# Performance work log

Measured on AMD Instinct MI355X. Metric: run time of the kernel, lower is better.

Reference implementation:

```python
import jax, jax.numpy as jnp
import numpy as np
from jax import lax

WINDOW_SIZE = 5
SIGMA = 1.0
DILATIONS = [1 + int(i ** 1.5) for i in range(5)]  # [1, 2, 3, 6, 9]
C1 = (0.01 * 255.0) ** 2
C2 = (0.03 * 255.0) ** 2


def _make_window(channel=1):
    x = np.arange(WINDOW_SIZE, dtype=np.float64)
    g = np.exp(-((x - WINDOW_SIZE // 2) ** 2) / (2.0 * SIGMA ** 2))
    g = g / g.sum()
    w2d = np.outer(g, g)
    w2d = w2d / w2d.sum()
    w = np.broadcast_to(w2d[None, None], (channel, 1, WINDOW_SIZE, WINDOW_SIZE))
    return jnp.asarray(w, jnp.float32)


def _dw_conv(x, window, dilation):
    # depthwise 'same' conv; pad = (dilated_kernel - 1)/2 = 2*dilation (always even total pad)
    pad = 2 * dilation
    return lax.conv_general_dilated(
        x, window, window_strides=(1, 1),
        padding=((pad, pad), (pad, pad)),
        rhs_dilation=(dilation, dilation),
        dimension_numbers=('NCHW', 'OIHW', 'NCHW'),
        feature_group_count=window.shape[0])


def _ssim_mean(img1, img2, window, dilation):
    mu1 = _dw_conv(img1, window, dilation)
    mu2 = _dw_conv(img2, window, dilation)
    si11 = _dw_conv(img1 * img1, window, dilation)
    si22 = _dw_conv(img2 * img2, window, dilation)
    si12 = _dw_conv(img1 * img2, window, dilation)
    mu1_sq = mu1 * mu1
    mu2_sq = mu2 * mu2
    mu1_mu2 = mu1 * mu2
    sigma1_sq = si11 - mu1_sq
    sigma2_sq = si22 - mu2_sq
    sigma12 = si12 - mu1_mu2
    ssim_map = ((2.0 * mu1_mu2 + C1) * (2.0 * sigma12 + C2)) / (
        (mu1_sq + mu2_sq + C1) * (sigma1_sq + sigma2_sq + C2))
    return jnp.mean(ssim_map)


def _avg_pool2(x):
    B, C, H, W = x.shape
    return x.reshape(B, C, H // 2, 2, W // 2, 2).mean(axis=(3, 5))


def setup_inputs() -> dict:
    key = jax.random.key(0)
    k1, k2 = jax.random.split(key)
    img1 = jax.random.uniform(k1, (16, 1, 1024, 1024), dtype=jnp.float32)
    img2 = jax.random.uniform(k2, (16, 1, 1024, 1024), dtype=jnp.float32)
    window = _make_window(channel=1)
    weights = jnp.asarray([0.0448, 0.2856, 0.3001, 0.2363, 0.1333], jnp.float32)
    return {"img1": img1, "img2": img2, "window": window, "weights": weights}


def reference(img1, img2, window, weights):
    eps = 1e-12
    m = jnp.max(img2)
    a = (img1 + eps) / (m + eps) * 255.0
    b = (img2 + eps) / (m + eps) * 255.0
    mssim = []
    for dil in DILATIONS:
        mssim.append(_ssim_mean(a, b, window, dil))
        a = _avg_pool2(a)
        b = _avg_pool2(b)
    mssim = jnp.stack(mssim)
    return 1.0 - jnp.prod(mssim ** weights)
```

## Files before the change

### kernel.cpp

```cpp
#include <hip/hip_runtime.h>
#include <math.h>

#define EPSN 1e-12f
#define SSIM_C1 6.5025f
#define SSIM_C2 58.5225f


typedef __attribute__((ext_vector_type(2))) float vf2;
typedef __attribute__((ext_vector_type(2))) _Float16 h2;
typedef __attribute__((ext_vector_type(8))) _Float16 h8;

__device__ __forceinline__ vf2 h2f(h2 v) { return vf2{(float)v.x, (float)v.y}; }


__global__ void init_ws_kernel(float* ws) {
    if (threadIdx.x < 16) ws[threadIdx.x] = 0.0f;
}


__global__ void max_kernel(const float4* __restrict__ img2, int n4,
                           unsigned* __restrict__ maxbits) {
    float m = 0.0f;
    for (int i = blockIdx.x * blockDim.x + threadIdx.x; i < n4;
         i += gridDim.x * blockDim.x) {
        float4 v = img2[i];
        m = fmaxf(fmaxf(m, fmaxf(v.x, v.y)), fmaxf(v.z, v.w));
    }
#pragma unroll
    for (int o = 32; o > 0; o >>= 1) m = fmaxf(m, __shfl_down(m, o));
    __shared__ float sm[4];
    int tid = threadIdx.x;
    if ((tid & 63) == 0) sm[tid >> 6] = m;
    __syncthreads();
    if (tid == 0) {
        float mm = fmaxf(fmaxf(sm[0], sm[1]), fmaxf(sm[2], sm[3]));
        atomicMax(maxbits, __float_as_uint(mm));
    }
}


__device__ __forceinline__ float ssim_px(vf2 vpm, vf2 vsq, float s2h) {
    float u = vpm.x * vpm.x, vv = vpm.y * vpm.y;
    float upv = u + vv, umv = u - vv;
    float qp = vsq.x + vsq.y, qm = vsq.x - vsq.y;
    float num1 = fmaf(s2h, umv, SSIM_C1);
    float den1 = fmaf(s2h, upv, SSIM_C1);
    float num2 = fmaf(s2h, qm - umv, SSIM_C2);
    float den2 = fmaf(s2h, qp - upv, SSIM_C2);
    return (num1 * num2) * __builtin_amdgcn_rcpf(den1 * den2);
}

__device__ __forceinline__ void load_g1(const float* __restrict__ window,
                                        float* g1) {
#pragma unroll
    for (int k = 0; k < 5; k++)
        g1[k] = ((window[k * 5 + 0] + window[k * 5 + 1]) +
                 (window[k * 5 + 2] + window[k * 5 + 3])) + window[k * 5 + 4];
}

__device__ __forceinline__ void block_sum_add(float local, float* part, int tid,
                                              float* __restrict__ sumOut) {
#pragma unroll
    for (int o = 32; o > 0; o >>= 1) local += __shfl_down(local, o);
    if ((tid & 63) == 0) part[tid >> 6] = local;
    __syncthreads();
    if (tid == 0)
        atomicAdd(sumOut, (part[0] + part[1]) + (part[2] + part[3]));
}

template <int D, int TPT, int LW, int L0>
__device__ __forceinline__ float sep_compute(const h2* AB, const float* g1,
                                             float s2h, int tx, int ty) {
    vf2 rPM[5], rSQ[5];
    float local = 0.0f;
    int rbase = ty * TPT;
#pragma unroll
    for (int ph = 0; ph < D; ++ph) {
        const int cnt = (TPT - ph + D - 1) / D;
#pragma unroll
        for (int k = 0; k < cnt + 4; ++k) {
            const h2* row = AB + (rbase + ph + k * D) * LW + (L0 - 2 * D) + tx;
            vf2 hpm = {0, 0}, hsq = {0, 0};
#pragma unroll
            for (int kt = 0; kt < 5; kt++) {
                vf2 f = h2f(row[kt * D]);
                vf2 w = g1[kt] * f;
                hpm += w;
                hsq += w * f;
            }
            rPM[k % 5] = hpm;
            rSQ[k % 5] = hsq;
            if (k >= 4) {
                vf2 vpm = {0, 0}, vsq = {0, 0};
#pragma unroll
                for (int kt = 0; kt < 5; kt++) {
                    int sl = (k - 4 + kt) % 5;
                    vpm += g1[kt] * rPM[sl];
                    vsq += g1[kt] * rSQ[sl];
                }
                local += ssim_px(vpm, vsq, s2h);
            }
        }
    }
    return local;
}

template <int D, int LH, int LW, int L0, int W>
__device__ __forceinline__ void stage_h2(const h2* __restrict__ base, h2* AB,
                                         int x0i, int y0, int tid) {
    for (int idx = tid; idx < LH * 16; idx += 256) {
        int ly = idx >> 4, j = idx & 15;
        int gy = y0 + ly;
        float4 g = make_float4(0, 0, 0, 0);
        if ((unsigned)gy < (unsigned)W)
            g = *(const float4*)(base + (size_t)gy * W + x0i + 4 * j);
        *(float4*)&AB[ly * LW + L0 + 4 * j] = g;
    }
    for (int idx = tid; idx < LH * 4 * D; idx += 256) {
        int ly = idx / (4 * D), h = idx % (4 * D);
        int gc = (h < 2 * D) ? h : h + 64;
        int gx = x0i - 2 * D + gc, gy = y0 + ly;
        h2 pm = {(_Float16)0.f, (_Float16)0.f};
        if ((unsigned)gx < (unsigned)W && (unsigned)gy < (unsigned)W)
            pm = base[(size_t)gy * W + gx];
        AB[ly * LW + (L0 - 2 * D) + gc] = pm;
    }
}


__global__ __launch_bounds__(256) void ssim0_kernel(
        const float* __restrict__ A, const float* __restrict__ B,
        const float* __restrict__ window, const unsigned* __restrict__ maxbits,
        float* __restrict__ sums, h2* __restrict__ pm1) {
    constexpr int TH = 64, TPT = 16, L0 = 4, LW = 72, LH = 68;
    __shared__ __align__(16) h2 AB[LH * LW];
    __shared__ float part[4];

    int tx = threadIdx.x, ty = threadIdx.y;
    int tid = ty * 64 + tx;
    int b = blockIdx.z;
    int x0i = blockIdx.x * 64;
    int y0 = blockIdx.y * TH - 2;

    const float* Ab = A + (size_t)b * 1024 * 1024;
    const float* Bb = B + (size_t)b * 1024 * 1024;
    for (int idx = tid; idx < LH * 16; idx += 256) {
        int ly = idx >> 4, j = idx & 15;
        int gy = y0 + ly;
        float4 a = make_float4(0, 0, 0, 0), v = make_float4(0, 0, 0, 0);
        if ((unsigned)gy < 1024u) {
            a = *(const float4*)(Ab + (size_t)gy * 1024 + x0i + 4 * j);
            v = *(const float4*)(Bb + (size_t)gy * 1024 + x0i + 4 * j);
        }
        h8 r;
        r[0] = (_Float16)(a.x + v.x); r[1] = (_Float16)(a.x - v.x);
        r[2] = (_Float16)(a.y + v.y); r[3] = (_Float16)(a.y - v.y);
        r[4] = (_Float16)(a.z + v.z); r[5] = (_Float16)(a.z - v.z);
        r[6] = (_Float16)(a.w + v.w); r[7] = (_Float16)(a.w - v.w);
        *(h8*)&AB[ly * LW + L0 + 4 * j] = r;
    }
    for (int idx = tid; idx < LH * 4; idx += 256) {
        int ly = idx >> 2, h = idx & 3;
        int gc = (h < 2) ? h : h + 64;
        int gx = x0i - 2 + gc, gy = y0 + ly;
        h2 pm = {(_Float16)0.f, (_Float16)0.f};
        if ((unsigned)gx < 1024u && (unsigned)gy < 1024u) {
            float a = Ab[(size_t)gy * 1024 + gx], v = Bb[(size_t)gy * 1024 + gx];
            pm = h2{(_Float16)(a + v), (_Float16)(a - v)};
        }
        AB[ly * LW + (L0 - 2) + gc] = pm;
    }
    __syncthreads();

    {
        int py = tid >> 3, j4 = tid & 7;
        const h2* r0 = AB + (2 + 2 * py) * LW + L0 + 8 * j4;
        const h2* r1 = r0 + LW;
        h2 q = {(_Float16)0.25f, (_Float16)0.25f};
        h8 o;
#pragma unroll
        for (int t = 0; t < 4; t++) {
            h2 s = ((r0[2 * t] + r0[2 * t + 1]) + (r1[2 * t] + r1[2 * t + 1])) * q;
            o[2 * t] = s.x; o[2 * t + 1] = s.y;
        }
        int gx = (x0i >> 1) + 4 * j4, gy = blockIdx.y * 32 + py;
        *(h8*)(pm1 + (size_t)b * 512 * 512 + (size_t)gy * 512 + gx) = o;
    }

    float g1[5];
    load_g1(window, g1);
    float mx = __uint_as_float(*maxbits);
    float sc = 255.0f / (mx + EPSN);
    float s2h = 0.5f * sc * sc;

    float local = sep_compute<1, TPT, LW, L0>(AB, g1, s2h, tx, ty);
    block_sum_add(local, part, tid, sums + 0);
}


__global__ __launch_bounds__(256) void ssim1_kernel(
        const h2* __restrict__ pm1, const float* __restrict__ window,
        const unsigned* __restrict__ maxbits, float* __restrict__ sums,
        h2* __restrict__ pm2, h2* __restrict__ pm3, h2* __restrict__ pm4) {
    constexpr int D = 2, TH = 64, TPT = 16, L0 = 4, LW = 72, LH = 72;
    __shared__ __align__(16) h2 AB[LH * LW];
    __shared__ float part[4];

    int tx = threadIdx.x, ty = threadIdx.y;
    int tid = ty * 64 + tx;
    int b = blockIdx.z, bx = blockIdx.x, by = blockIdx.y;
    int x0i = bx * 64, y0 = by * TH - 4;
    const h2* base = pm1 + (size_t)b * 512 * 512;

    stage_h2<D, LH, LW, L0, 512>(base, AB, x0i, y0, tid);
    __syncthreads();

    {
        int py = tid >> 3, j4 = tid & 7;
        const h2* r0 = AB + (4 + 2 * py) * LW + 4 + 8 * j4;
        const h2* r1 = r0 + LW;
        h2 q = {(_Float16)0.25f, (_Float16)0.25f};
        h8 o;
#pragma unroll
        for (int t = 0; t < 4; t++) {
            h2 s = ((r0[2 * t] + r0[2 * t + 1]) + (r1[2 * t] + r1[2 * t + 1])) * q;
            o[2 * t] = s.x; o[2 * t + 1] = s.y;
        }
        int gx = bx * 32 + 4 * j4, gy = by * 32 + py;
        *(h8*)(pm2 + (size_t)b * 256 * 256 + (size_t)gy * 256 + gx) = o;
    }
    {
        int py = tid >> 4, px = tid & 15;
        h2 acc = {(_Float16)0.f, (_Float16)0.f};
#pragma unroll
        for (int ry = 0; ry < 4; ry++)
#pragma unroll
            for (int rx = 0; rx < 4; rx++)
                acc += AB[(4 + 4 * py + ry) * LW + 4 + 4 * px + rx];
        h2 q = {(_Float16)0.0625f, (_Float16)0.0625f};
        acc *= q;
        pm3[(size_t)b * 128 * 128 + (size_t)(by * 16 + py) * 128 + bx * 16 + px] = acc;
    }
    if (tid < 64) {
        int py = tid >> 3, px = tid & 7;
        h2 acc = {(_Float16)0.f, (_Float16)0.f};
#pragma unroll
        for (int ry = 0; ry < 8; ry++)
#pragma unroll
            for (int rx = 0; rx < 8; rx++)
                acc += AB[(4 + 8 * py + ry) * LW + 4 + 8 * px + rx];
        h2 q = {(_Float16)0.015625f, (_Float16)0.015625f};
        acc *= q;
        pm4[(size_t)b * 64 * 64 + (size_t)(by * 8 + py) * 64 + bx * 8 + px] = acc;
    }

    float g1[5];
    load_g1(window, g1);
    float mx = __uint_as_float(*maxbits);
    float sc = 255.0f / (mx + EPSN);
    float s2h = 0.5f * sc * sc;

    float local = sep_compute<D, TPT, LW, L0>(AB, g1, s2h, tx, ty);
    block_sum_add(local, part, tid, sums + 1);
}


template <int D, int TW, int TH, int W, int LW, int LH>
__device__ void direct_level(const h2* __restrict__ base, const float* g1,
                             int bx, int by, float s2h, float* part,
                             float* __restrict__ sumOut, h2* AB, int tid) {
    constexpr int NOUT = TW * TH / 256;
    int x0 = bx * TW - 2 * D, y0 = by * TH - 2 * D;

    for (int idx = tid; idx < LW * LH; idx += 256) {
        int ly = idx / LW, lx = idx - ly * LW;
        int px = x0 + lx, py = y0 + ly;
        h2 pm = {(_Float16)0.f, (_Float16)0.f};
        if ((unsigned)px < (unsigned)W && (unsigned)py < (unsigned)W)
            pm = base[(size_t)py * W + px];
        AB[idx] = pm;
    }
    __syncthreads();

    vf2 mu[NOUT], sq[NOUT];
#pragma unroll
    for (int j = 0; j < NOUT; j++) { mu[j] = vf2{0, 0}; sq[j] = vf2{0, 0}; }
#pragma unroll
    for (int ky = 0; ky < 5; ky++) {
#pragma unroll
        for (int kx = 0; kx < 5; kx++) {
            float w = g1[ky] * g1[kx];
#pragma unroll
            for (int j = 0; j < NOUT; j++) {
                int lin = tid + j * 256;
                int ox = lin % TW, oy = lin / TW;
                vf2 f = h2f(AB[(oy + ky * D) * LW + ox + kx * D]);
                vf2 wf = w * f;
                mu[j] += wf;
                sq[j] += wf * f;
            }
        }
    }
    float local = 0.0f;
#pragma unroll
    for (int j = 0; j < NOUT; j++) local += ssim_px(mu[j], sq[j], s2h);
    block_sum_add(local, part, tid, sumOut);
}

__global__ __launch_bounds__(256) void tail_kernel(
        const h2* __restrict__ pm2, const h2* __restrict__ pm3,
        const h2* __restrict__ pm4, const float* __restrict__ window,
        const unsigned* __restrict__ maxbits, float* __restrict__ sums,
        unsigned* __restrict__ counter, const float* __restrict__ weights,
        unsigned* __restrict__ out) {
    extern __shared__ __align__(16) h2 ldsdyn[];
    __shared__ float part[4];
    int tid = threadIdx.x;

    float g1[5];
    load_g1(window, g1);
    float mx = __uint_as_float(*maxbits);
    float sc = 255.0f / (mx + EPSN);
    float s2h = 0.5f * sc * sc;

    int bid = blockIdx.x;
    if (bid < 512) {
        int b = bid >> 5, r = bid & 31, by = r >> 2, bx = r & 3;
        constexpr int D = 3, TPT = 8, L0 = 8, LW = 80, LH = 44;
        const h2* base = pm2 + (size_t)b * 256 * 256;
        stage_h2<D, LH, LW, L0, 256>(base, ldsdyn, bx * 64, by * 32 - 6, tid);
        __syncthreads();
        float local = sep_compute<D, TPT, LW, L0>(ldsdyn, g1, s2h,
                                                  tid & 63, tid >> 6);
        block_sum_add(local, part, tid, sums + 2);
    } else if (bid < 768) {
        int t = bid - 512, b = t >> 4, r = t & 15, by = r >> 1, bx = r & 1;
        const h2* base = pm3 + (size_t)b * 128 * 128;
        direct_level<6, 64, 16, 128, 88, 40>(base, g1, bx, by, s2h, part,
                                             sums + 3, ldsdyn, tid);
    } else {
        int t = bid - 768, b = t >> 3, r = t & 7, by = r >> 1, bx = r & 1;
        const h2* base = pm4 + (size_t)b * 64 * 64;
        direct_level<9, 32, 16, 64, 68, 52>(base, g1, bx, by, s2h, part,
                                            sums + 4, ldsdyn, tid);
    }

    if (tid == 0) {
        __threadfence();
        if (atomicAdd(counter, 1u) == 895u) {
            __threadfence();
            const float counts[5] = {16.0f * 1024 * 1024, 16.0f * 512 * 512,
                                     16.0f * 256 * 256,   16.0f * 128 * 128,
                                     16.0f * 64 * 64};
            float prod = 1.0f;
#pragma unroll
            for (int i = 0; i < 5; i++) {
                float m = atomicAdd(sums + i, 0.0f) / counts[i];
                prod *= powf(m, weights[i]);
            }
            float r = 1.0f - prod;
            unsigned bits = __float_as_uint(r);
            unsigned lsb = (bits >> 16) & 1u;
            unsigned hi = (bits + 0x7FFFu + lsb) >> 16;
            out[0] = (hi << 16) | hi;
        }
    }
}


extern "C" void kernel_launch(void* const* d_in, const int* in_sizes, int n_in,
                              void* d_out, int out_size, void* d_ws, size_t ws_size,
                              hipStream_t stream) {
    const float* img1 = (const float*)d_in[0];
    const float* img2 = (const float*)d_in[1];
    const float* window = (const float*)d_in[2];
    const float* weights = (const float*)d_in[3];

    float* ws = (float*)d_ws;
    unsigned* maxbits = (unsigned*)d_ws;
    float* sums = ws + 4;
    unsigned* counter = (unsigned*)(ws + 10);
    size_t off = 512;
    h2* pm1 = (h2*)(ws + off); off += (size_t)16 * 512 * 512;
    h2* pm2 = (h2*)(ws + off); off += (size_t)16 * 256 * 256;
    h2* pm3 = (h2*)(ws + off); off += (size_t)16 * 128 * 128;
    h2* pm4 = (h2*)(ws + off); off += (size_t)16 * 64 * 64;

    init_ws_kernel<<<1, 64, 0, stream>>>(ws);
    max_kernel<<<2048, 256, 0, stream>>>((const float4*)img2,
                                         16 * 1024 * 1024 / 4, maxbits);
    ssim0_kernel<<<dim3(16, 16, 16), dim3(64, 4), 0, stream>>>(
        img1, img2, window, maxbits, sums, pm1);
    ssim1_kernel<<<dim3(8, 8, 16), dim3(64, 4), 0, stream>>>(
        pm1, window, maxbits, sums, pm2, pm3, pm4);
    tail_kernel<<<896, 256, 14144, stream>>>(pm2, pm3, pm4, window, maxbits,
                                             sums, counter, weights,
                                             (unsigned*)d_out);
}
```

Baseline: 279.1 us.

## Register-block separable SSIM with packed fp16 horizontal pass and smaller tiles

Replaces the per-thread column-strip separable convolution with a 4-column by 2-row register-blocked version. Each thread loads a row span with 16-byte LDS reads and does the horizontal 5-tap filter in packed fp16 (h2) arithmetic. It then scatters the results into fp32 vertical accumulators. Tile heights are halved (64→32 rows), doubling grid size, and LDS padding/offsets are adjusted. The intent is fewer LDS loads and packed-math throughput, at the cost of more halo overhead and reduced fp16 precision in the horizontal sums (including squared terms).

```diff
diff --git a/kernel.cpp b/kernel.cpp
--- a/kernel.cpp
+++ b/kernel.cpp
@@ -8,7 +8,9 @@
 
 typedef __attribute__((ext_vector_type(2))) float vf2;
 typedef __attribute__((ext_vector_type(2))) _Float16 h2;
+typedef __attribute__((ext_vector_type(4))) _Float16 h4;
 typedef __attribute__((ext_vector_type(8))) _Float16 h8;
+typedef __attribute__((ext_vector_type(4))) unsigned int u32x4;
 
 __device__ __forceinline__ vf2 h2f(h2 v) { return vf2{(float)v.x, (float)v.y}; }
 
@@ -51,11 +53,13 @@
 }
 
 __device__ __forceinline__ void load_g1(const float* __restrict__ window,
-                                        float* g1) {
-#pragma unroll
-    for (int k = 0; k < 5; k++)
+                                        float* g1, h2* g1h) {
+#pragma unroll
+    for (int k = 0; k < 5; k++) {
         g1[k] = ((window[k * 5 + 0] + window[k * 5 + 1]) +
                  (window[k * 5 + 2] + window[k * 5 + 3])) + window[k * 5 + 4];
+        g1h[k] = h2{(_Float16)g1[k], (_Float16)g1[k]};
+    }
 }
 
 __device__ __forceinline__ void block_sum_add(float local, float* part, int tid,
@@ -68,40 +72,70 @@
         atomicAdd(sumOut, (part[0] + part[1]) + (part[2] + part[3]));
 }
 
-template <int D, int TPT, int LW, int L0>
-__device__ __forceinline__ float sep_compute(const h2* AB, const float* g1,
-                                             float s2h, int tx, int ty) {
-    vf2 rPM[5], rSQ[5];
+template <int D, int RPT, int LW, int L0>
+__device__ __forceinline__ float sep4_compute(const h2* AB, const float* g1,
+                                              const h2* g1h, float s2h,
+                                              int cg, int rg) {
+    constexpr int SPAN = 4 * D + 4;
+    constexpr int NW = SPAN / 4;
+    constexpr int NIR = RPT + 4 * D;
+
+    vf2 apm[RPT][4], asq[RPT][4];
+#pragma unroll
+    for (int j = 0; j < RPT; j++)
+#pragma unroll
+        for (int c = 0; c < 4; c++) {
+            apm[j][c] = vf2{0.f, 0.f};
+            asq[j][c] = vf2{0.f, 0.f};
+        }
+
+    const h2* base = AB + (L0 - 2 * D) + 4 * cg + (rg * RPT) * LW;
+#pragma unroll
+    for (int i = 0; i < NIR; i++) {
+        h2 f[SPAN];
+#pragma unroll
+        for (int w = 0; w < NW; w++) {
+            u32x4 q = *(const u32x4*)(base + i * LW + 4 * w);
+            f[4 * w + 0] = __builtin_bit_cast(h2, q.x);
+            f[4 * w + 1] = __builtin_bit_cast(h2, q.y);
+            f[4 * w + 2] = __builtin_bit_cast(h2, q.z);
+            f[4 * w + 3] = __builtin_bit_cast(h2, q.w);
+        }
+        h2 f2[SPAN];
+#pragma unroll
+        for (int j = 0; j < SPAN; j++) f2[j] = f[j] * f[j];
+
+        vf2 HP[4], HQ[4];
+#pragma unroll
+        for (int c = 0; c < 4; c++) {
+            h2 hp = g1h[0] * f[c];
+            h2 hq = g1h[0] * f2[c];
+#pragma unroll
+            for (int kt = 1; kt < 5; kt++) {
+                hp += g1h[kt] * f[c + kt * D];
+                hq += g1h[kt] * f2[c + kt * D];
+            }
+            HP[c] = h2f(hp);
+            HQ[c] = h2f(hq);
+        }
+#pragma unroll
+        for (int kt = 0; kt < 5; kt++) {
+            const int j = i - kt * D;
+            if (j >= 0 && j < RPT) {
+#pragma unroll
+                for (int c = 0; c < 4; c++) {
+                    apm[j][c] += g1[kt] * HP[c];
+                    asq[j][c] += g1[kt] * HQ[c];
+                }
+            }
+        }
+    }
     float local = 0.0f;
-    int rbase = ty * TPT;
-#pragma unroll
-    for (int ph = 0; ph < D; ++ph) {
-        const int cnt = (TPT - ph + D - 1) / D;
-#pragma unroll
-        for (int k = 0; k < cnt + 4; ++k) {
-            const h2* row = AB + (rbase + ph + k * D) * LW + (L0 - 2 * D) + tx;
-            vf2 hpm = {0, 0}, hsq = {0, 0};
-#pragma unroll
-            for (int kt = 0; kt < 5; kt++) {
-                vf2 f = h2f(row[kt * D]);
-                vf2 w = g1[kt] * f;
-                hpm += w;
-                hsq += w * f;
-            }
-            rPM[k % 5] = hpm;
-            rSQ[k % 5] = hsq;
-            if (k >= 4) {
-                vf2 vpm = {0, 0}, vsq = {0, 0};
-#pragma unroll
-                for (int kt = 0; kt < 5; kt++) {
-                    int sl = (k - 4 + kt) % 5;
-                    vpm += g1[kt] * rPM[sl];
-                    vsq += g1[kt] * rSQ[sl];
-                }
-                local += ssim_px(vpm, vsq, s2h);
-            }
-        }
-    }
+#pragma unroll
+    for (int j = 0; j < RPT; j++)
+#pragma unroll
+        for (int c = 0; c < 4; c++)
+            local += ssim_px(apm[j][c], asq[j][c], s2h);
     return local;
 }
 
@@ -114,7 +148,14 @@
         float4 g = make_float4(0, 0, 0, 0);
         if ((unsigned)gy < (unsigned)W)
             g = *(const float4*)(base + (size_t)gy * W + x0i + 4 * j);
-        *(float4*)&AB[ly * LW + L0 + 4 * j] = g;
+        h2* p = &AB[ly * LW + L0 + 4 * j];
+        if constexpr ((L0 & 3) == 2) {
+            h8 r = __builtin_bit_cast(h8, g);
+            *(h4*)p = h4{r[0], r[1], r[2], r[3]};
+            *(h4*)(p + 2) = h4{r[4], r[5], r[6], r[7]};
+        } else {
+            *(float4*)p = g;
+        }
     }
     for (int idx = tid; idx < LH * 4 * D; idx += 256) {
         int ly = idx / (4 * D), h = idx % (4 * D);
@@ -132,7 +173,7 @@
         const float* __restrict__ A, const float* __restrict__ B,
         const float* __restrict__ window, const unsigned* __restrict__ maxbits,
         float* __restrict__ sums, h2* __restrict__ pm1) {
-    constexpr int TH = 64, TPT = 16, L0 = 4, LW = 72, LH = 68;
+    constexpr int TH = 32, RPT = 2, L0 = 2, LW = 68, LH = 36;
     __shared__ __align__(16) h2 AB[LH * LW];
     __shared__ float part[4];
 
@@ -157,7 +198,9 @@
         r[2] = (_Float16)(a.y + v.y); r[3] = (_Float16)(a.y - v.y);
         r[4] = (_Float16)(a.z + v.z); r[5] = (_Float16)(a.z - v.z);
         r[6] = (_Float16)(a.w + v.w); r[7] = (_Float16)(a.w - v.w);
-        *(h8*)&AB[ly * LW + L0 + 4 * j] = r;
+        h2* p = &AB[ly * LW + L0 + 4 * j];
+        *(h4*)p = h4{r[0], r[1], r[2], r[3]};
+        *(h4*)(p + 2) = h4{r[4], r[5], r[6], r[7]};
     }
     for (int idx = tid; idx < LH * 4; idx += 256) {
         int ly = idx >> 2, h = idx & 3;
@@ -172,7 +215,7 @@
     }
     __syncthreads();
 
-    {
+    if (tid < 128) {
         int py = tid >> 3, j4 = tid & 7;
         const h2* r0 = AB + (2 + 2 * py) * LW + L0 + 8 * j4;
         const h2* r1 = r0 + LW;
@@ -183,17 +226,18 @@
             h2 s = ((r0[2 * t] + r0[2 * t + 1]) + (r1[2 * t] + r1[2 * t + 1])) * q;
             o[2 * t] = s.x; o[2 * t + 1] = s.y;
         }
-        int gx = (x0i >> 1) + 4 * j4, gy = blockIdx.y * 32 + py;
+        int gx = (x0i >> 1) + 4 * j4, gy = blockIdx.y * 16 + py;
         *(h8*)(pm1 + (size_t)b * 512 * 512 + (size_t)gy * 512 + gx) = o;
     }
 
-    float g1[5];
-    load_g1(window, g1);
+    float g1[5]; h2 g1h[5];
+    load_g1(window, g1, g1h);
     float mx = __uint_as_float(*maxbits);
     float sc = 255.0f / (mx + EPSN);
     float s2h = 0.5f * sc * sc;
 
-    float local = sep_compute<1, TPT, LW, L0>(AB, g1, s2h, tx, ty);
+    float local = sep4_compute<1, RPT, LW, L0>(AB, g1, g1h, s2h,
+                                               tid & 15, tid >> 4);
     block_sum_add(local, part, tid, sums + 0);
 }
 
@@ -202,7 +246,7 @@
         const h2* __restrict__ pm1, const float* __restrict__ window,
         const unsigned* __restrict__ maxbits, float* __restrict__ sums,
         h2* __restrict__ pm2, h2* __restrict__ pm3, h2* __restrict__ pm4) {
-    constexpr int D = 2, TH = 64, TPT = 16, L0 = 4, LW = 72, LH = 72;
+    constexpr int D = 2, TH = 32, RPT = 2, L0 = 4, LW = 76, LH = 40;
     __shared__ __align__(16) h2 AB[LH * LW];
     __shared__ float part[4];
 
@@ -215,7 +259,7 @@
     stage_h2<D, LH, LW, L0, 512>(base, AB, x0i, y0, tid);
     __syncthreads();
 
-    {
+    if (tid < 128) {
         int py = tid >> 3, j4 = tid & 7;
         const h2* r0 = AB + (4 + 2 * py) * LW + 4 + 8 * j4;
         const h2* r1 = r0 + LW;
@@ -226,10 +270,10 @@
             h2 s = ((r0[2 * t] + r0[2 * t + 1]) + (r1[2 * t] + r1[2 * t + 1])) * q;
             o[2 * t] = s.x; o[2 * t + 1] = s.y;
         }
-        int gx = bx * 32 + 4 * j4, gy = by * 32 + py;
+        int gx = bx * 32 + 4 * j4, gy = by * 16 + py;
         *(h8*)(pm2 + (size_t)b * 256 * 256 + (size_t)gy * 256 + gx) = o;
     }
-    {
+    if (tid < 128) {
         int py = tid >> 4, px = tid & 15;
         h2 acc = {(_Float16)0.f, (_Float16)0.f};
 #pragma unroll
@@ -239,9 +283,9 @@
                 acc += AB[(4 + 4 * py + ry) * LW + 4 + 4 * px + rx];
         h2 q = {(_Float16)0.0625f, (_Float16)0.0625f};
         acc *= q;
-        pm3[(size_t)b * 128 * 128 + (size_t)(by * 16 + py) * 128 + bx * 16 + px] = acc;
-    }
-    if (tid < 64) {
+        pm3[(size_t)b * 128 * 128 + (size_t)(by * 8 + py) * 128 + bx * 16 + px] = acc;
+    }
+    if (tid < 32) {
         int py = tid >> 3, px = tid & 7;
         h2 acc = {(_Float16)0.f, (_Float16)0.f};
 #pragma unroll
@@ -251,16 +295,17 @@
                 acc += AB[(4 + 8 * py + ry) * LW + 4 + 8 * px + rx];
         h2 q = {(_Float16)0.015625f, (_Float16)0.015625f};
         acc *= q;
-        pm4[(size_t)b * 64 * 64 + (size_t)(by * 8 + py) * 64 + bx * 8 + px] = acc;
-    }
-
-    float g1[5];
-    load_g1(window, g1);
+        pm4[(size_t)b * 64 * 64 + (size_t)(by * 4 + py) * 64 + bx * 8 + px] = acc;
+    }
+
+    float g1[5]; h2 g1h[5];
+    load_g1(window, g1, g1h);
     float mx = __uint_as_float(*maxbits);
     float sc = 255.0f / (mx + EPSN);
     float s2h = 0.5f * sc * sc;
 
-    float local = sep_compute<D, TPT, LW, L0>(AB, g1, s2h, tx, ty);
+    float local = sep4_compute<D, RPT, LW, L0>(AB, g1, g1h, s2h,
+                                               tid & 15, tid >> 4);
     block_sum_add(local, part, tid, sums + 1);
 }
 
@@ -317,8 +362,8 @@
     __shared__ float part[4];
     int tid = threadIdx.x;
 
-    float g1[5];
-    load_g1(window, g1);
+    float g1[5]; h2 g1h[5];
+    load_g1(window, g1, g1h);
     float mx = __uint_as_float(*maxbits);
     float sc = 255.0f / (mx + EPSN);
     float s2h = 0.5f * sc * sc;
@@ -326,12 +371,12 @@
     int bid = blockIdx.x;
     if (bid < 512) {
         int b = bid >> 5, r = bid & 31, by = r >> 2, bx = r & 3;
-        constexpr int D = 3, TPT = 8, L0 = 8, LW = 80, LH = 44;
+        constexpr int D = 3, RPT = 2, L0 = 6, LW = 76, LH = 44;
         const h2* base = pm2 + (size_t)b * 256 * 256;
         stage_h2<D, LH, LW, L0, 256>(base, ldsdyn, bx * 64, by * 32 - 6, tid);
         __syncthreads();
-        float local = sep_compute<D, TPT, LW, L0>(ldsdyn, g1, s2h,
-                                                  tid & 63, tid >> 6);
+        float local = sep4_compute<D, RPT, LW, L0>(ldsdyn, g1, g1h, s2h,
+                                                   tid & 15, tid >> 4);
         block_sum_add(local, part, tid, sums + 2);
     } else if (bid < 768) {
         int t = bid - 512, b = t >> 4, r = t & 15, by = r >> 1, bx = r & 1;
@@ -389,9 +434,9 @@
     init_ws_kernel<<<1, 64, 0, stream>>>(ws);
     max_kernel<<<2048, 256, 0, stream>>>((const float4*)img2,
                                          16 * 1024 * 1024 / 4, maxbits);
-    ssim0_kernel<<<dim3(16, 16, 16), dim3(64, 4), 0, stream>>>(
+    ssim0_kernel<<<dim3(16, 32, 16), dim3(64, 4), 0, stream>>>(
         img1, img2, window, maxbits, sums, pm1);
-    ssim1_kernel<<<dim3(8, 8, 16), dim3(64, 4), 0, stream>>>(
+    ssim1_kernel<<<dim3(8, 16, 16), dim3(64, 4), 0, stream>>>(
         pm1, window, maxbits, sums, pm2, pm3, pm4);
     tail_kernel<<<896, 256, 14144, stream>>>(pm2, pm3, pm4, window, maxbits,
                                              sums, counter, weights,
```

After: 330.8 us. +18.5%, slower.
